# Optimization experiments

Measured on AMD Instinct MI355X. Metric: run time of the kernel, lower is better.

Reference implementation:

```python
import jax, jax.numpy as jnp
import numpy as np

NUM_HEADS = 16
DIM = 1024
B, L = 2, 2048
NEG = -10000000000.0


def setup_inputs() -> dict:
    key = jax.random.key(0)
    ks = jax.random.split(key, 8)
    queries = jax.random.normal(ks[0], (B, L, DIM), dtype=jnp.float32)
    keys = jax.random.normal(ks[1], (B, L, DIM), dtype=jnp.float32)
    values = jax.random.normal(ks[2], (B, L, DIM), dtype=jnp.float32)
    mask = jax.random.uniform(ks[3], (B, L, L)) < 0.1
    s = 1.0 / np.sqrt(DIM)
    Wq = jax.random.uniform(ks[4], (DIM, DIM), minval=-s, maxval=s, dtype=jnp.float32)
    Wk = jax.random.uniform(ks[5], (DIM, DIM), minval=-s, maxval=s, dtype=jnp.float32)
    Wv = jax.random.uniform(ks[6], (DIM, DIM), minval=-s, maxval=s, dtype=jnp.float32)
    Wo = jax.random.uniform(ks[7], (DIM, DIM), minval=-s, maxval=s, dtype=jnp.float32)
    return {"queries": queries, "keys": keys, "values": values, "mask": mask,
            "Wq": Wq, "Wk": Wk, "Wv": Wv, "Wo": Wo}


def reference(queries, keys, values, mask, Wq, Wk, Wv, Wo):
    b, l, d = queries.shape
    h = NUM_HEADS
    dk = d // h
    # torch Linear(bias=False): y = x @ W.T ; then view(b, l, dk, h) -> head axis LAST
    qs = (queries @ Wq.T).reshape(b, l, dk, h)
    ks = (keys @ Wk.T).reshape(b, l, dk, h)
    vs = (values @ Wv.T).reshape(b, l, dk, h)
    # routing is None in the live code path
    w = jnp.einsum('bidh,bodh->bioh', qs, ks) / jnp.sqrt(jnp.asarray(dk, jnp.float32))
    w = jnp.where(mask[..., None], NEG, w)          # masked_fill where mask True
    w = jax.nn.softmax(w, axis=-2)                   # softmax over key axis 'o'
    mha = jnp.einsum('bioh,bodh->bidh', w, vs).reshape(b, l, d)
    # dropout is identity in eval mode
    return mha @ Wo.T
```

## Files before the change

kernel.cpp:

```cpp
#include <hip/hip_runtime.h>
#include <hip/hip_bf16.h>
#include <cstdint>
#include <cstddef>

typedef unsigned short ushort_t;
typedef __attribute__((ext_vector_type(8))) short short8;
typedef __attribute__((ext_vector_type(8))) unsigned short ushort8;
typedef __attribute__((ext_vector_type(4))) unsigned short ushort4v;
typedef __attribute__((ext_vector_type(4))) float f32x4;
typedef __attribute__((ext_vector_type(2))) unsigned long long ull2;
typedef __attribute__((ext_vector_type(2))) unsigned int uint2v;

#define LPAD 72

#define PIPE_WAIT_BAR(N) do {                                              \
    asm volatile("s_waitcnt vmcnt(" #N ") lgkmcnt(0)" ::: "memory");       \
    __builtin_amdgcn_s_barrier();                                          \
    asm volatile("" ::: "memory");                                         \
} while (0)

__device__ __forceinline__ unsigned short f2bf(float f) {
    unsigned int x = __float_as_uint(f);
    unsigned int r = x + 0x7fffu + ((x >> 16) & 1u);
    return (unsigned short)(r >> 16);
}

__device__ __forceinline__ unsigned int cvt_pk_bf16(float lo, float hi) {
    unsigned int r;
    asm("v_cvt_pk_bf16_f32 %0, %1, %2" : "=v"(r) : "v"(lo), "v"(hi));
    return r;
}

__device__ __forceinline__ void async16(const ushort_t* g, ushort_t* l) {
    __builtin_amdgcn_global_load_lds(
        (const __attribute__((address_space(1))) unsigned int*)g,
        (__attribute__((address_space(3))) unsigned int*)l,
        16, 0, 0);
}

__global__ __launch_bounds__(256) void cvt(const float* __restrict__ q,
                                           const float* __restrict__ k,
                                           const float* __restrict__ v,
                                           const float* __restrict__ Wq,
                                           const float* __restrict__ Wk,
                                           const float* __restrict__ Wv,
                                           ushort_t* __restrict__ qb,
                                           ushort_t* __restrict__ kb,
                                           ushort_t* __restrict__ vb,
                                           ushort_t* __restrict__ Wqb,
                                           ushort_t* __restrict__ Wkb,
                                           ushort_t* __restrict__ Wvb) {
    const int z = blockIdx.y;
    const float* X = (z == 0) ? q : (z == 1) ? k : v;
    const float* W = (z == 0) ? Wq : (z == 1) ? Wk : Wv;
    ushort_t* Xo = (z == 0) ? qb : (z == 1) ? kb : vb;
    ushort_t* Wo2 = (z == 0) ? Wqb : (z == 1) ? Wkb : Wvb;
    const size_t idx = (((size_t)blockIdx.x << 8) + threadIdx.x) << 3;
    const float* src; ushort_t* dst; float sc = 1.0f;
    if (idx < 4194304) { src = X + idx; dst = Xo + idx; if (z == 0) sc = 0.125f; }
    else               { src = W + (idx - 4194304); dst = Wo2 + (idx - 4194304); }
    f32x4 a0 = *(const f32x4*)src, a1 = *(const f32x4*)(src + 4);
    ushort8 o;
    #pragma unroll
    for (int j = 0; j < 4; j++) { o[j] = f2bf(a0[j] * sc); o[j + 4] = f2bf(a1[j] * sc); }
    *(ushort8*)dst = o;
}

__global__ __launch_bounds__(256) void maskbits_kernel(const int* __restrict__ mask,
                                                       unsigned long long* __restrict__ Mbits) {
    const int row  = blockIdx.x;
    const int w    = threadIdx.x >> 6;
    const int lane = threadIdx.x & 63;
    const int* mrow = mask + (size_t)row * 2048;
    #pragma unroll
    for (int it = 0; it < 8; it++) {
        const int o = (it << 8) + (w << 6) + lane;
        const unsigned long long bb = __ballot(mrow[o] != 0);
        if (lane == 0) Mbits[(size_t)((it << 2) + w) * 4096 + row] = bb;
    }
}

__global__ __launch_bounds__(256) void woswz(const float* __restrict__ W,
                                             ushort_t* __restrict__ WoH) {
    __shared__ float row[1024 + 64];
    const int j = blockIdx.x, t = threadIdx.x;
    f32x4 v = *(const f32x4*)(W + (size_t)j * 1024 + (t << 2));
    #pragma unroll
    for (int s = 0; s < 4; s++) { const int c = (t << 2) + s; row[c + (c >> 4)] = v[s]; }
    __syncthreads();
    #pragma unroll
    for (int s = 0; s < 4; s++) {
        const int k = t + (s << 8);
        const int col = ((k & 63) << 4) + (k >> 6);
        WoH[(size_t)j * 1024 + k] = f2bf(row[col + (col >> 4)]);
    }
}

__global__ __launch_bounds__(256) void gemm_proj(const ushort_t* __restrict__ qb,
                                                 const ushort_t* __restrict__ kb,
                                                 const ushort_t* __restrict__ vb,
                                                 const ushort_t* __restrict__ Wqb,
                                                 const ushort_t* __restrict__ Wkb,
                                                 const ushort_t* __restrict__ Wvb,
                                                 ushort_t* __restrict__ Qh,
                                                 ushort_t* __restrict__ Kh,
                                                 ushort_t* __restrict__ VhT) {
    __shared__ ushort_t Xs[3][4096];
    __shared__ ushort_t Ws[3][4096];

    const int lid  = blockIdx.x;
    const int nIdx = lid / 96;
    const int rem  = lid % 96;
    const int z    = rem >> 5;
    const int mIdx = rem & 31;
    const int n0   = nIdx << 7;
    const int m0   = mIdx << 7;

    const ushort_t* Xb = (z == 0) ? qb : (z == 1) ? kb : vb;
    const ushort_t* Wb = (z == 0) ? Wqb : (z == 1) ? Wkb : Wvb;

    const int tid  = threadIdx.x;
    const int w    = tid >> 6;
    const int lane = tid & 63;
    const int lm   = lane & 15;
    const int quad = lane >> 4;
    const int wm   = w & 1;
    const int wn   = w >> 1;

    f32x4 acc[4][4];
    #pragma unroll
    for (int i = 0; i < 4; i++)
        #pragma unroll
        for (int j = 0; j < 4; j++) acc[i][j] = (f32x4){0.f, 0.f, 0.f, 0.f};

    auto stage = [&](int k0, int buf) {
        #pragma unroll
        for (int i = 0; i < 2; i++) {
            const int L   = (((w << 1) + i) << 6) + lane;
            const int c4  = L >> 7, row = L & 127;
            const int lb  = (((w << 1) + i) << 6) << 3;
            async16(Xb + (size_t)(m0 + row) * 1024 + k0 + (c4 << 3), &Xs[buf][lb]);
            async16(Wb + (size_t)(n0 + row) * 1024 + k0 + (c4 << 3), &Ws[buf][lb]);
        }
    };

    stage(0, 0);
    stage(32, 1);
    PIPE_WAIT_BAR(4);

    int cur = 0;
    for (int t = 0; t < 32; ++t) {
        int nb = cur + 2; if (nb >= 3) nb -= 3;
        if (t < 30) stage((t + 2) << 5, nb);
        short8 af[4], bf4[4];
        #pragma unroll
        for (int mf = 0; mf < 4; mf++)
            af[mf] = *(const short8*)&Xs[cur][((quad << 7) + (wm << 6) + (mf << 4) + lm) << 3];
        #pragma unroll
        for (int nf = 0; nf < 4; nf++)
            bf4[nf] = *(const short8*)&Ws[cur][((quad << 7) + (wn << 6) + (nf << 4) + lm) << 3];
        #pragma unroll
        for (int mf = 0; mf < 4; mf++)
            #pragma unroll
            for (int nf = 0; nf < 4; nf++)
                acc[mf][nf] = __builtin_amdgcn_mfma_f32_16x16x32_bf16(af[mf], bf4[nf], acc[mf][nf], 0, 0, 0);
        if (t < 30)       PIPE_WAIT_BAR(4);
        else if (t == 30) PIPE_WAIT_BAR(0);
        cur += 1; if (cur == 3) cur = 0;
    }

    const int bb    = m0 >> 11;
    const int l0    = m0 & 2047;
    const int dbase = (n0 >> 4) + (wn << 2);
    if (z != 2) {
        ushort_t* OUT = (z == 0) ? Qh : Kh;
        #pragma unroll
        for (int mf = 0; mf < 4; mf++)
            #pragma unroll
            for (int r = 0; r < 4; r++) {
                const int row = (wm << 6) + (mf << 4) + (quad << 2) + r;
                ushort4v o = { f2bf(acc[mf][0][r]), f2bf(acc[mf][1][r]),
                               f2bf(acc[mf][2][r]), f2bf(acc[mf][3][r]) };
                *(ushort4v*)(OUT + ((size_t)((bb << 4) + lm) * 2048 + l0 + row) * 64 + dbase) = o;
            }
    } else {
        #pragma unroll
        for (int mf = 0; mf < 4; mf++)
            #pragma unroll
            for (int nf = 0; nf < 4; nf++) {
                const int lbase = l0 + (wm << 6) + (mf << 4) + (quad << 2);
                ushort4v o = { f2bf(acc[mf][nf][0]), f2bf(acc[mf][nf][1]),
                               f2bf(acc[mf][nf][2]), f2bf(acc[mf][nf][3]) };
                *(ushort4v*)(VhT + ((size_t)((bb << 4) + lm) * 64 + dbase + nf) * 2048 + lbase) = o;
            }
    }
}

__global__ __launch_bounds__(256) void gemm_out(const ushort_t* __restrict__ mhaH,
                                                const ushort_t* __restrict__ WoH,
                                                float* __restrict__ C) {
    __shared__ ushort_t Xs[3][4096];
    __shared__ ushort_t Ws[3][2048];

    const int lid  = blockIdx.x;
    const int mIdx = ((lid & 7) << 2) | ((lid >> 3) & 3);
    const int nIdx = lid >> 5;
    const int m0   = mIdx << 7;
    const int n0   = nIdx << 6;

    const int tid  = threadIdx.x;
    const int w    = tid >> 6;
    const int lane = tid & 63;
    const int lm   = lane & 15;
    const int quad = lane >> 4;
    const int wm   = w & 1;
    const int wn   = w >> 1;
    const int ab   = m0 >> 11;
    const int al0  = m0 & 2047;

    f32x4 acc[4][2];
    #pragma unroll
    for (int i = 0; i < 4; i++)
        #pragma unroll
        for (int j = 0; j < 2; j++) acc[i][j] = (f32x4){0.f, 0.f, 0.f, 0.f};

    auto stage = [&](int k0, int buf) {
        const int h  = k0 >> 6;
        const int d0 = k0 & 63;
        #pragma unroll
        for (int i = 0; i < 2; i++) {
            const int L   = (i << 8) + (w << 6) + lane;
            const int c4  = L >> 7, row = L & 127;
            async16(mhaH + ((size_t)(ab * 16 + h) * 2048 + al0 + row) * 64 + d0 + (c4 << 3),
                    &Xs[buf][((i << 8) + (w << 6)) << 3]);
        }
        {
            const int L   = (w << 6) + lane;
            const int c4  = L >> 6, row = L & 63;
            async16(WoH + (size_t)(n0 + row) * 1024 + k0 + (c4 << 3),
                    &Ws[buf][(w << 6) << 3]);
        }
    };

    stage(0, 0);
    stage(32, 1);
    PIPE_WAIT_BAR(3);

    int cur = 0;
    for (int t = 0; t < 32; ++t) {
        int nb = cur + 2; if (nb >= 3) nb -= 3;
        if (t < 30) stage((t + 2) << 5, nb);
        short8 af[4], bf2[2];
        #pragma unroll
        for (int mf = 0; mf < 4; mf++)
            af[mf] = *(const short8*)&Xs[cur][((quad << 7) + (wm << 6) + (mf << 4) + lm) << 3];
        #pragma unroll
        for (int nf = 0; nf < 2; nf++)
            bf2[nf] = *(const short8*)&Ws[cur][((quad << 6) + (wn << 5) + (nf << 4) + lm) << 3];
        #pragma unroll
        for (int mf = 0; mf < 4; mf++)
            #pragma unroll
            for (int nf = 0; nf < 2; nf++)
                acc[mf][nf] = __builtin_amdgcn_mfma_f32_16x16x32_bf16(af[mf], bf2[nf], acc[mf][nf], 0, 0, 0);
        if (t < 30)       PIPE_WAIT_BAR(3);
        else if (t == 30) PIPE_WAIT_BAR(0);
        cur += 1; if (cur == 3) cur = 0;
    }
    #pragma unroll
    for (int mf = 0; mf < 4; mf++)
        #pragma unroll
        for (int nf = 0; nf < 2; nf++)
            #pragma unroll
            for (int r = 0; r < 4; r++) {
                const int row = m0 + (wm << 6) + (mf << 4) + (quad << 2) + r;
                const int col = n0 + (wn << 5) + (nf << 4) + lm;
                C[(size_t)row * 1024 + col] = acc[mf][nf][r];
            }
}

__global__ __launch_bounds__(256, 2) void flash_attn(const ushort_t* __restrict__ Qh,
                                                     const ushort_t* __restrict__ Kh,
                                                     const ushort_t* __restrict__ VhT,
                                                     const unsigned long long* __restrict__ Mbits,
                                                     ushort_t* __restrict__ mhaH) {
    __shared__ ushort_t Ks[3][4096];
    __shared__ ushort_t Vs[3][4096];
    __shared__ ushort_t Pw[4][2][16 * LPAD];

    const int tid  = threadIdx.x;
    const int w    = tid >> 6;
    const int lane = tid & 63;
    const int lm   = lane & 15;
    const int quad = lane >> 4;
    const int lid  = blockIdx.x;
    const int bh   = ((lid & 7) << 2) | ((lid >> 3) & 3);
    const int q0   = (lid >> 5) << 7;
    const int b    = bh >> 4;

    const ushort_t* Qb  = Qh  + ((size_t)bh << 17);
    const ushort_t* Kb  = Kh  + ((size_t)bh << 17);
    const ushort_t* Vtb = VhT + ((size_t)bh << 17);

    short8 aq[2][2];
    #pragma unroll
    for (int g = 0; g < 2; g++) {
        const ushort_t* qp = Qb + (size_t)(q0 + (w << 5) + (g << 4) + lm) * 64 + (quad << 3);
        aq[g][0] = *(const short8*)qp;
        aq[g][1] = *(const short8*)(qp + 32);
    }

    float l_part[2][4] = {{0.f,0.f,0.f,0.f},{0.f,0.f,0.f,0.f}};
    f32x4 o_acc[2][4] = {{{0.f,0.f,0.f,0.f},{0.f,0.f,0.f,0.f},{0.f,0.f,0.f,0.f},{0.f,0.f,0.f,0.f}},
                         {{0.f,0.f,0.f,0.f},{0.f,0.f,0.f,0.f},{0.f,0.f,0.f,0.f},{0.f,0.f,0.f,0.f}}};

    const int rowbase  = (b << 11) + q0 + (w << 5);
    const int shamt    = (lm & 7) << 2;
    const bool hi_half = lm >= 8;

    const ushort_t* ksrc = Kb  + (size_t)((lm << 2) + w) * 64 + (quad << 3);
    const ushort_t* vsrc = Vtb + (size_t)((w << 4) + lm) * 2048 + (quad << 3);

    auto stageKV = [&](int kt0, int buf) {
        async16(ksrc + (size_t)kt0 * 64,      &Ks[buf][((w << 7)     ) << 3]);
        async16(ksrc + (size_t)kt0 * 64 + 32, &Ks[buf][((w << 7) + 64) << 3]);
        async16(vsrc + kt0,      &Vs[buf][((w << 7)     ) << 3]);
        async16(vsrc + kt0 + 32, &Vs[buf][((w << 7) + 64) << 3]);
    };

    stageKV(0, 0);
    stageKV(64, 1);
    PIPE_WAIT_BAR(4);

    int cur = 0;
    for (int t = 0; t < 32; ++t) {
        const int kt0 = t << 6;
        int nb = cur + 2; if (nb >= 3) nb -= 3;

        const unsigned long long* Mt = Mbits + (size_t)(kt0 >> 6) * 4096 + rowbase;
        unsigned long long mb[2][4];
        #pragma unroll
        for (int g = 0; g < 2; g++) {
            const unsigned long long* mp = Mt + (g << 4) + (quad << 2);
            ull2 t0 = *(const ull2*)mp;
            ull2 t1 = *(const ull2*)(mp + 2);
            mb[g][0] = t0[0]; mb[g][1] = t0[1]; mb[g][2] = t1[0]; mb[g][3] = t1[1];
        }

        if (t < 30) stageKV(kt0 + 128, nb);

        short8 bk[4][2], bv[4][2];
        #pragma unroll
        for (int c = 0; c < 4; c++) {
            bk[c][0] = *(const short8*)&Ks[cur][((c << 7) + lane) << 3];
            bk[c][1] = *(const short8*)&Ks[cur][((c << 7) + 64 + lane) << 3];
            bv[c][0] = *(const short8*)&Vs[cur][((c << 7) + lane) << 3];
            bv[c][1] = *(const short8*)&Vs[cur][((c << 7) + 64 + lane) << 3];
        }

        f32x4 s[2][4];
        __builtin_amdgcn_s_setprio(1);
        #pragma unroll
        for (int g = 0; g < 2; g++)
            #pragma unroll
            for (int c = 0; c < 4; c++) {
                f32x4 zz = {0.f, 0.f, 0.f, 0.f};
                zz = __builtin_amdgcn_mfma_f32_16x16x32_bf16(aq[g][0], bk[c][0], zz, 0, 0, 0);
                zz = __builtin_amdgcn_mfma_f32_16x16x32_bf16(aq[g][1], bk[c][1], zz, 0, 0, 0);
                s[g][c] = zz;
            }
        __builtin_amdgcn_s_setprio(0);

        #pragma unroll
        for (int g = 0; g < 2; g++) {
            #pragma unroll
            for (int r = 0; r < 4; r++) {
                const unsigned long long m64 = mb[g][r];
                const unsigned word = hi_half ? (unsigned)(m64 >> 32) : (unsigned)m64;
                const unsigned nib  = (word >> shamt) & 0xFu;
                float p0 = __expf(s[g][0][r]); if (nib & 1u) p0 = 0.f;
                float p1 = __expf(s[g][1][r]); if (nib & 2u) p1 = 0.f;
                float p2 = __expf(s[g][2][r]); if (nib & 4u) p2 = 0.f;
                float p3 = __expf(s[g][3][r]); if (nib & 8u) p3 = 0.f;
                l_part[g][r] += (p0 + p1) + (p2 + p3);
                uint2v pv2;
                pv2[0] = cvt_pk_bf16(p0, p1);
                pv2[1] = cvt_pk_bf16(p2, p3);
                *(uint2v*)&Pw[w][g][((quad << 2) + r) * LPAD + (lm << 2)] = pv2;
            }
        }

        __builtin_amdgcn_s_setprio(1);
        #pragma unroll
        for (int g = 0; g < 2; g++) {
            short8 ap0 = *(const short8*)&Pw[w][g][lm * LPAD + (quad << 3)];
            short8 ap1 = *(const short8*)&Pw[w][g][lm * LPAD + 32 + (quad << 3)];
            #pragma unroll
            for (int cd = 0; cd < 4; cd++) {
                o_acc[g][cd] = __builtin_amdgcn_mfma_f32_16x16x32_bf16(ap0, bv[cd][0], o_acc[g][cd], 0, 0, 0);
                o_acc[g][cd] = __builtin_amdgcn_mfma_f32_16x16x32_bf16(ap1, bv[cd][1], o_acc[g][cd], 0, 0, 0);
            }
        }
        __builtin_amdgcn_s_setprio(0);

        if (t < 30)       PIPE_WAIT_BAR(4);
        else if (t == 30) PIPE_WAIT_BAR(0);
        cur += 1; if (cur == 3) cur = 0;
    }

    #pragma unroll
    for (int g = 0; g < 2; g++) {
        #pragma unroll
        for (int r = 0; r < 4; r++) {
            float l = l_part[g][r];
            l += __shfl_xor(l, 1, 64);
            l += __shfl_xor(l, 2, 64);
            l += __shfl_xor(l, 4, 64);
            l += __shfl_xor(l, 8, 64);
            const float inv_l = 1.0f / l;
            const int i = q0 + (w << 5) + (g << 4) + (quad << 2) + r;
            ushort_t* orow = mhaH + (((size_t)bh * 2048 + i) << 6);
            #pragma unroll
            for (int cd = 0; cd < 4; cd++)
                orow[(cd << 4) + lm] = f2bf(o_acc[g][cd][r] * inv_l);
        }
    }
}

extern "C" void kernel_launch(void* const* d_in, const int* in_sizes, int n_in,
                              void* d_out, int out_size, void* d_ws, size_t ws_size,
                              hipStream_t stream) {
    const float* q    = (const float*)d_in[0];
    const float* k    = (const float*)d_in[1];
    const float* v    = (const float*)d_in[2];
    const int*   mask = (const int*)d_in[3];
    const float* Wq   = (const float*)d_in[4];
    const float* Wk   = (const float*)d_in[5];
    const float* Wv   = (const float*)d_in[6];
    const float* Wo   = (const float*)d_in[7];
    float* out = (float*)d_out;

    ushort_t* qb   = (ushort_t*)d_ws;
    ushort_t* kb   = qb  + 4194304;
    ushort_t* vb   = kb  + 4194304;
    ushort_t* Wqb  = vb  + 4194304;
    ushort_t* Wkb  = Wqb + 1048576;
    ushort_t* Wvb  = Wkb + 1048576;
    ushort_t* Qh   = Wvb + 1048576;
    ushort_t* Kh   = Qh  + 4194304;
    ushort_t* VhT  = Kh  + 4194304;
    ushort_t* mhaH = qb;
    ushort_t* WoH  = kb;
    unsigned long long* Mbits = (unsigned long long*)(kb + 1048576);

    dim3 gb(256);
    cvt<<<dim3(2560, 3), gb, 0, stream>>>(q, k, v, Wq, Wk, Wv, qb, kb, vb, Wqb, Wkb, Wvb);
    gemm_proj<<<dim3(768), gb, 0, stream>>>(qb, kb, vb, Wqb, Wkb, Wvb, Qh, Kh, VhT);
    maskbits_kernel<<<dim3(4096), gb, 0, stream>>>(mask, Mbits);
    woswz<<<dim3(1024), gb, 0, stream>>>(Wo, WoH);
    flash_attn<<<dim3(512), gb, 0, stream>>>(Qh, Kh, VhT, Mbits, mhaH);
    gemm_out<<<dim3(512), gb, 0, stream>>>(mhaH, WoH, out);
}
```

Baseline: 311.7 us.

## Fuse fp32-to-bf16 activation conversion into projection GEMM and merge prep kernels

```diff
diff --git a/kernel.cpp b/kernel.cpp
--- a/kernel.cpp
+++ b/kernel.cpp
@@ -38,74 +38,66 @@
         16, 0, 0);
 }
 
-__global__ __launch_bounds__(256) void cvt(const float* __restrict__ q,
-                                           const float* __restrict__ k,
-                                           const float* __restrict__ v,
-                                           const float* __restrict__ Wq,
-                                           const float* __restrict__ Wk,
-                                           const float* __restrict__ Wv,
-                                           ushort_t* __restrict__ qb,
-                                           ushort_t* __restrict__ kb,
-                                           ushort_t* __restrict__ vb,
-                                           ushort_t* __restrict__ Wqb,
-                                           ushort_t* __restrict__ Wkb,
-                                           ushort_t* __restrict__ Wvb) {
-    const int z = blockIdx.y;
-    const float* X = (z == 0) ? q : (z == 1) ? k : v;
-    const float* W = (z == 0) ? Wq : (z == 1) ? Wk : Wv;
-    ushort_t* Xo = (z == 0) ? qb : (z == 1) ? kb : vb;
-    ushort_t* Wo2 = (z == 0) ? Wqb : (z == 1) ? Wkb : Wvb;
-    const size_t idx = (((size_t)blockIdx.x << 8) + threadIdx.x) << 3;
-    const float* src; ushort_t* dst; float sc = 1.0f;
-    if (idx < 4194304) { src = X + idx; dst = Xo + idx; if (z == 0) sc = 0.125f; }
-    else               { src = W + (idx - 4194304); dst = Wo2 + (idx - 4194304); }
-    f32x4 a0 = *(const f32x4*)src, a1 = *(const f32x4*)(src + 4);
-    ushort8 o;
-    #pragma unroll
-    for (int j = 0; j < 4; j++) { o[j] = f2bf(a0[j] * sc); o[j + 4] = f2bf(a1[j] * sc); }
-    *(ushort8*)dst = o;
-}
-
-__global__ __launch_bounds__(256) void maskbits_kernel(const int* __restrict__ mask,
-                                                       unsigned long long* __restrict__ Mbits) {
-    const int row  = blockIdx.x;
-    const int w    = threadIdx.x >> 6;
-    const int lane = threadIdx.x & 63;
-    const int* mrow = mask + (size_t)row * 2048;
-    #pragma unroll
-    for (int it = 0; it < 8; it++) {
-        const int o = (it << 8) + (w << 6) + lane;
-        const unsigned long long bb = __ballot(mrow[o] != 0);
-        if (lane == 0) Mbits[(size_t)((it << 2) + w) * 4096 + row] = bb;
-    }
-}
-
-__global__ __launch_bounds__(256) void woswz(const float* __restrict__ W,
-                                             ushort_t* __restrict__ WoH) {
-    __shared__ float row[1024 + 64];
-    const int j = blockIdx.x, t = threadIdx.x;
-    f32x4 v = *(const f32x4*)(W + (size_t)j * 1024 + (t << 2));
-    #pragma unroll
-    for (int s = 0; s < 4; s++) { const int c = (t << 2) + s; row[c + (c >> 4)] = v[s]; }
-    __syncthreads();
-    #pragma unroll
-    for (int s = 0; s < 4; s++) {
-        const int k = t + (s << 8);
-        const int col = ((k & 63) << 4) + (k >> 6);
-        WoH[(size_t)j * 1024 + k] = f2bf(row[col + (col >> 4)]);
-    }
-}
-
-__global__ __launch_bounds__(256) void gemm_proj(const ushort_t* __restrict__ qb,
-                                                 const ushort_t* __restrict__ kb,
-                                                 const ushort_t* __restrict__ vb,
+__global__ __launch_bounds__(256) void prep(const int* __restrict__ mask,
+                                            const float* __restrict__ Wq,
+                                            const float* __restrict__ Wk,
+                                            const float* __restrict__ Wv,
+                                            const float* __restrict__ Wo,
+                                            ushort_t* __restrict__ Wqb,
+                                            ushort_t* __restrict__ Wkb,
+                                            ushort_t* __restrict__ Wvb,
+                                            ushort_t* __restrict__ WoH,
+                                            unsigned long long* __restrict__ Mbits) {
+    __shared__ float srow[1024 + 64];
+    const int bid = blockIdx.x;
+    const int tid = threadIdx.x;
+    if (bid < 4096) {
+        const int row  = bid;
+        const int w    = tid >> 6;
+        const int lane = tid & 63;
+        const int* mrow = mask + (size_t)row * 2048;
+        #pragma unroll
+        for (int it = 0; it < 8; it++) {
+            const int o = (it << 8) + (w << 6) + lane;
+            const unsigned long long bb = __ballot(mrow[o] != 0);
+            if (lane == 0) Mbits[(size_t)((it << 2) + w) * 4096 + row] = bb;
+        }
+    } else if (bid < 5632) {
+        const int q    = bid - 4096;
+        const int wsel = q >> 9;
+        const float* W = (wsel == 0) ? Wq : (wsel == 1) ? Wk : Wv;
+        ushort_t* Wb   = (wsel == 0) ? Wqb : (wsel == 1) ? Wkb : Wvb;
+        const size_t idx = (((size_t)(q & 511) << 8) + tid) << 3;
+        f32x4 a0 = *(const f32x4*)(W + idx), a1 = *(const f32x4*)(W + idx + 4);
+        ushort8 o;
+        #pragma unroll
+        for (int j = 0; j < 4; j++) { o[j] = f2bf(a0[j]); o[j + 4] = f2bf(a1[j]); }
+        *(ushort8*)(Wb + idx) = o;
+    } else {
+        const int j = bid - 5632;
+        f32x4 v = *(const f32x4*)(Wo + (size_t)j * 1024 + (tid << 2));
+        #pragma unroll
+        for (int s = 0; s < 4; s++) { const int c = (tid << 2) + s; srow[c + (c >> 4)] = v[s]; }
+        __syncthreads();
+        #pragma unroll
+        for (int s = 0; s < 4; s++) {
+            const int k = tid + (s << 8);
+            const int col = ((k & 63) << 4) + (k >> 6);
+            WoH[(size_t)j * 1024 + k] = f2bf(srow[col + (col >> 4)]);
+        }
+    }
+}
+
+__global__ __launch_bounds__(256) void gemm_proj(const float* __restrict__ qf,
+                                                 const float* __restrict__ kf,
+                                                 const float* __restrict__ vf,
                                                  const ushort_t* __restrict__ Wqb,
                                                  const ushort_t* __restrict__ Wkb,
                                                  const ushort_t* __restrict__ Wvb,
                                                  ushort_t* __restrict__ Qh,
                                                  ushort_t* __restrict__ Kh,
                                                  ushort_t* __restrict__ VhT) {
-    __shared__ ushort_t Xs[3][4096];
+    __shared__ ushort_t Xs[2][4096];
     __shared__ ushort_t Ws[3][4096];
 
     const int lid  = blockIdx.x;
@@ -116,8 +108,9 @@
     const int n0   = nIdx << 7;
     const int m0   = mIdx << 7;
 
-    const ushort_t* Xb = (z == 0) ? qb : (z == 1) ? kb : vb;
+    const float* Xf = (z == 0) ? qf : (z == 1) ? kf : vf;
     const ushort_t* Wb = (z == 0) ? Wqb : (z == 1) ? Wkb : Wvb;
+    const float sc = (z == 0) ? 0.125f : 1.0f;
 
     const int tid  = threadIdx.x;
     const int w    = tid >> 6;
@@ -133,40 +126,71 @@
         #pragma unroll
         for (int j = 0; j < 4; j++) acc[i][j] = (f32x4){0.f, 0.f, 0.f, 0.f};
 
-    auto stage = [&](int k0, int buf) {
+    const float* xbase = Xf + (size_t)(m0 + lane) * 1024 + (w << 3);
+
+    auto loadX = [&](int k0, f32x4 xr[2][2]) {
         #pragma unroll
         for (int i = 0; i < 2; i++) {
-            const int L   = (((w << 1) + i) << 6) + lane;
-            const int c4  = L >> 7, row = L & 127;
-            const int lb  = (((w << 1) + i) << 6) << 3;
-            async16(Xb + (size_t)(m0 + row) * 1024 + k0 + (c4 << 3), &Xs[buf][lb]);
+            const float* sp = xbase + (size_t)(i << 6) * 1024 + k0;
+            xr[i][0] = *(const f32x4*)sp;
+            xr[i][1] = *(const f32x4*)(sp + 4);
+        }
+    };
+    auto writeX = [&](const f32x4 xr[2][2], int buf) {
+        #pragma unroll
+        for (int i = 0; i < 2; i++) {
+            ushort8 o;
+            #pragma unroll
+            for (int j = 0; j < 4; j++) {
+                o[j]     = f2bf(xr[i][0][j] * sc);
+                o[j + 4] = f2bf(xr[i][1][j] * sc);
+            }
+            const int L = (w << 7) + (i << 6) + lane;
+            *(ushort8*)&Xs[buf][L << 3] = o;
+        }
+    };
+    auto stageW = [&](int k0, int buf) {
+        #pragma unroll
+        for (int i = 0; i < 2; i++) {
+            const int L  = (((w << 1) + i) << 6) + lane;
+            const int c4 = L >> 7, row = L & 127;
+            const int lb = (((w << 1) + i) << 6) << 3;
             async16(Wb + (size_t)(n0 + row) * 1024 + k0 + (c4 << 3), &Ws[buf][lb]);
         }
     };
 
-    stage(0, 0);
-    stage(32, 1);
-    PIPE_WAIT_BAR(4);
-
-    int cur = 0;
+    {
+        f32x4 x0[2][2];
+        loadX(0, x0);
+        stageW(0, 0);
+        stageW(32, 1);
+        writeX(x0, 0);
+        PIPE_WAIT_BAR(2);
+    }
+
+    int wcur = 0;
     for (int t = 0; t < 32; ++t) {
-        int nb = cur + 2; if (nb >= 3) nb -= 3;
-        if (t < 30) stage((t + 2) << 5, nb);
+        f32x4 xr[2][2];
+        if (t < 31) loadX((t + 1) << 5, xr);
+        if (t < 30) { int nb = wcur + 2; if (nb >= 3) nb -= 3; stageW((t + 2) << 5, nb); }
+
         short8 af[4], bf4[4];
         #pragma unroll
         for (int mf = 0; mf < 4; mf++)
-            af[mf] = *(const short8*)&Xs[cur][((quad << 7) + (wm << 6) + (mf << 4) + lm) << 3];
+            af[mf] = *(const short8*)&Xs[t & 1][((quad << 7) + (wm << 6) + (mf << 4) + lm) << 3];
         #pragma unroll
         for (int nf = 0; nf < 4; nf++)
-            bf4[nf] = *(const short8*)&Ws[cur][((quad << 7) + (wn << 6) + (nf << 4) + lm) << 3];
+            bf4[nf] = *(const short8*)&Ws[wcur][((quad << 7) + (wn << 6) + (nf << 4) + lm) << 3];
         #pragma unroll
         for (int mf = 0; mf < 4; mf++)
             #pragma unroll
             for (int nf = 0; nf < 4; nf++)
                 acc[mf][nf] = __builtin_amdgcn_mfma_f32_16x16x32_bf16(af[mf], bf4[nf], acc[mf][nf], 0, 0, 0);
-        if (t < 30)       PIPE_WAIT_BAR(4);
+
+        if (t < 31) writeX(xr, (t + 1) & 1);
+        if (t < 30)       PIPE_WAIT_BAR(2);
         else if (t == 30) PIPE_WAIT_BAR(0);
-        cur += 1; if (cur == 3) cur = 0;
+        wcur += 1; if (wcur == 3) wcur = 0;
     }
 
     const int bb    = m0 >> 11;
@@ -439,24 +463,19 @@
     const float* Wo   = (const float*)d_in[7];
     float* out = (float*)d_out;
 
-    ushort_t* qb   = (ushort_t*)d_ws;
-    ushort_t* kb   = qb  + 4194304;
-    ushort_t* vb   = kb  + 4194304;
-    ushort_t* Wqb  = vb  + 4194304;
+    ushort_t* Wqb  = (ushort_t*)d_ws;
     ushort_t* Wkb  = Wqb + 1048576;
     ushort_t* Wvb  = Wkb + 1048576;
-    ushort_t* Qh   = Wvb + 1048576;
+    ushort_t* WoH  = Wvb + 1048576;
+    unsigned long long* Mbits = (unsigned long long*)(WoH + 1048576);
+    ushort_t* Qh   = WoH + 1048576 + 524288;
     ushort_t* Kh   = Qh  + 4194304;
     ushort_t* VhT  = Kh  + 4194304;
-    ushort_t* mhaH = qb;
-    ushort_t* WoH  = kb;
-    unsigned long long* Mbits = (unsigned long long*)(kb + 1048576);
+    ushort_t* mhaH = VhT + 4194304;
 
     dim3 gb(256);
-    cvt<<<dim3(2560, 3), gb, 0, stream>>>(q, k, v, Wq, Wk, Wv, qb, kb, vb, Wqb, Wkb, Wvb);
-    gemm_proj<<<dim3(768), gb, 0, stream>>>(qb, kb, vb, Wqb, Wkb, Wvb, Qh, Kh, VhT);
-    maskbits_kernel<<<dim3(4096), gb, 0, stream>>>(mask, Mbits);
-    woswz<<<dim3(1024), gb, 0, stream>>>(Wo, WoH);
+    prep<<<dim3(6656), gb, 0, stream>>>(mask, Wq, Wk, Wv, Wo, Wqb, Wkb, Wvb, WoH, Mbits);
+    gemm_proj<<<dim3(768), gb, 0, stream>>>(q, k, v, Wqb, Wkb, Wvb, Qh, Kh, VhT);
     flash_attn<<<dim3(512), gb, 0, stream>>>(Qh, Kh, VhT, Mbits, mhaH);
     gemm_out<<<dim3(512), gb, 0, stream>>>(mhaH, WoH, out);
 }
```

Measured after the change: 326.6 us. 1.05x slower.

## Enlarge projection GEMM tiles to 256x256 and merge prep kernels

Applied to the files above, without the earlier changes.

```diff
diff --git a/kernel.cpp b/kernel.cpp
--- a/kernel.cpp
+++ b/kernel.cpp
@@ -38,27 +38,35 @@
         16, 0, 0);
 }
 
-__global__ __launch_bounds__(256) void cvt(const float* __restrict__ q,
-                                           const float* __restrict__ k,
-                                           const float* __restrict__ v,
-                                           const float* __restrict__ Wq,
-                                           const float* __restrict__ Wk,
-                                           const float* __restrict__ Wv,
-                                           ushort_t* __restrict__ qb,
-                                           ushort_t* __restrict__ kb,
-                                           ushort_t* __restrict__ vb,
-                                           ushort_t* __restrict__ Wqb,
-                                           ushort_t* __restrict__ Wkb,
-                                           ushort_t* __restrict__ Wvb) {
-    const int z = blockIdx.y;
-    const float* X = (z == 0) ? q : (z == 1) ? k : v;
-    const float* W = (z == 0) ? Wq : (z == 1) ? Wk : Wv;
-    ushort_t* Xo = (z == 0) ? qb : (z == 1) ? kb : vb;
-    ushort_t* Wo2 = (z == 0) ? Wqb : (z == 1) ? Wkb : Wvb;
-    const size_t idx = (((size_t)blockIdx.x << 8) + threadIdx.x) << 3;
+__global__ __launch_bounds__(256) void prep1(const float* __restrict__ q,
+                                             const float* __restrict__ k,
+                                             const float* __restrict__ v,
+                                             const float* __restrict__ Wq,
+                                             const float* __restrict__ Wk,
+                                             const float* __restrict__ Wv,
+                                             ushort_t* __restrict__ qb,
+                                             ushort_t* __restrict__ kb,
+                                             ushort_t* __restrict__ vb,
+                                             ushort_t* __restrict__ Wqb,
+                                             ushort_t* __restrict__ Wkb,
+                                             ushort_t* __restrict__ Wvb) {
+    const int bid = blockIdx.x;
+    const int tid = threadIdx.x;
     const float* src; ushort_t* dst; float sc = 1.0f;
-    if (idx < 4194304) { src = X + idx; dst = Xo + idx; if (z == 0) sc = 0.125f; }
-    else               { src = W + (idx - 4194304); dst = Wo2 + (idx - 4194304); }
+    if (bid < 6144) {
+        const int z   = bid >> 11;
+        const int blk = bid & 2047;
+        const size_t idx = (((size_t)blk << 8) + tid) << 3;
+        src = ((z == 0) ? q : (z == 1) ? k : v) + idx;
+        dst = ((z == 0) ? qb : (z == 1) ? kb : vb) + idx;
+        if (z == 0) sc = 0.125f;
+    } else {
+        const int qq   = bid - 6144;
+        const int wsel = qq >> 9;
+        const size_t idx = (((size_t)(qq & 511) << 8) + tid) << 3;
+        src = ((wsel == 0) ? Wq : (wsel == 1) ? Wk : Wv) + idx;
+        dst = ((wsel == 0) ? Wqb : (wsel == 1) ? Wkb : Wvb) + idx;
+    }
     f32x4 a0 = *(const f32x4*)src, a1 = *(const f32x4*)(src + 4);
     ushort8 o;
     #pragma unroll
@@ -66,55 +74,58 @@
     *(ushort8*)dst = o;
 }
 
-__global__ __launch_bounds__(256) void maskbits_kernel(const int* __restrict__ mask,
-                                                       unsigned long long* __restrict__ Mbits) {
-    const int row  = blockIdx.x;
-    const int w    = threadIdx.x >> 6;
-    const int lane = threadIdx.x & 63;
-    const int* mrow = mask + (size_t)row * 2048;
-    #pragma unroll
-    for (int it = 0; it < 8; it++) {
-        const int o = (it << 8) + (w << 6) + lane;
-        const unsigned long long bb = __ballot(mrow[o] != 0);
-        if (lane == 0) Mbits[(size_t)((it << 2) + w) * 4096 + row] = bb;
-    }
-}
-
-__global__ __launch_bounds__(256) void woswz(const float* __restrict__ W,
-                                             ushort_t* __restrict__ WoH) {
-    __shared__ float row[1024 + 64];
-    const int j = blockIdx.x, t = threadIdx.x;
-    f32x4 v = *(const f32x4*)(W + (size_t)j * 1024 + (t << 2));
-    #pragma unroll
-    for (int s = 0; s < 4; s++) { const int c = (t << 2) + s; row[c + (c >> 4)] = v[s]; }
-    __syncthreads();
-    #pragma unroll
-    for (int s = 0; s < 4; s++) {
-        const int k = t + (s << 8);
-        const int col = ((k & 63) << 4) + (k >> 6);
-        WoH[(size_t)j * 1024 + k] = f2bf(row[col + (col >> 4)]);
-    }
-}
-
-__global__ __launch_bounds__(256) void gemm_proj(const ushort_t* __restrict__ qb,
-                                                 const ushort_t* __restrict__ kb,
-                                                 const ushort_t* __restrict__ vb,
-                                                 const ushort_t* __restrict__ Wqb,
-                                                 const ushort_t* __restrict__ Wkb,
-                                                 const ushort_t* __restrict__ Wvb,
-                                                 ushort_t* __restrict__ Qh,
-                                                 ushort_t* __restrict__ Kh,
-                                                 ushort_t* __restrict__ VhT) {
-    __shared__ ushort_t Xs[3][4096];
-    __shared__ ushort_t Ws[3][4096];
+__global__ __launch_bounds__(256) void prep2(const int* __restrict__ mask,
+                                             const float* __restrict__ Wo,
+                                             ushort_t* __restrict__ WoH,
+                                             unsigned long long* __restrict__ Mbits) {
+    __shared__ float srow[1024 + 64];
+    const int bid = blockIdx.x;
+    const int tid = threadIdx.x;
+    if (bid < 4096) {
+        const int row  = bid;
+        const int w    = tid >> 6;
+        const int lane = tid & 63;
+        const int* mrow = mask + (size_t)row * 2048;
+        #pragma unroll
+        for (int it = 0; it < 8; it++) {
+            const int o = (it << 8) + (w << 6) + lane;
+            const unsigned long long bb = __ballot(mrow[o] != 0);
+            if (lane == 0) Mbits[(size_t)((it << 2) + w) * 4096 + row] = bb;
+        }
+    } else {
+        const int j = bid - 4096;
+        f32x4 v = *(const f32x4*)(Wo + (size_t)j * 1024 + (tid << 2));
+        #pragma unroll
+        for (int s = 0; s < 4; s++) { const int c = (tid << 2) + s; srow[c + (c >> 4)] = v[s]; }
+        __syncthreads();
+        #pragma unroll
+        for (int s = 0; s < 4; s++) {
+            const int k = tid + (s << 8);
+            const int col = ((k & 63) << 4) + (k >> 6);
+            WoH[(size_t)j * 1024 + k] = f2bf(srow[col + (col >> 4)]);
+        }
+    }
+}
+
+__global__ __launch_bounds__(512, 2) void gemm_proj(const ushort_t* __restrict__ qb,
+                                                    const ushort_t* __restrict__ kb,
+                                                    const ushort_t* __restrict__ vb,
+                                                    const ushort_t* __restrict__ Wqb,
+                                                    const ushort_t* __restrict__ Wkb,
+                                                    const ushort_t* __restrict__ Wvb,
+                                                    ushort_t* __restrict__ Qh,
+                                                    ushort_t* __restrict__ Kh,
+                                                    ushort_t* __restrict__ VhT) {
+    __shared__ ushort_t Xs[3][8192];
+    __shared__ ushort_t Ws[3][8192];
 
     const int lid  = blockIdx.x;
-    const int nIdx = lid / 96;
-    const int rem  = lid % 96;
-    const int z    = rem >> 5;
-    const int mIdx = rem & 31;
-    const int n0   = nIdx << 7;
-    const int m0   = mIdx << 7;
+    const int nIdx = lid / 48;
+    const int rem  = lid % 48;
+    const int z    = rem >> 4;
+    const int mIdx = rem & 15;
+    const int n0   = nIdx << 8;
+    const int m0   = mIdx << 8;
 
     const ushort_t* Xb = (z == 0) ? qb : (z == 1) ? kb : vb;
     const ushort_t* Wb = (z == 0) ? Wqb : (z == 1) ? Wkb : Wvb;
@@ -127,9 +138,9 @@
     const int wm   = w & 1;
     const int wn   = w >> 1;
 
-    f32x4 acc[4][4];
-    #pragma unroll
-    for (int i = 0; i < 4; i++)
+    f32x4 acc[8][4];
+    #pragma unroll
+    for (int i = 0; i < 8; i++)
         #pragma unroll
         for (int j = 0; j < 4; j++) acc[i][j] = (f32x4){0.f, 0.f, 0.f, 0.f};
 
@@ -137,7 +148,7 @@
         #pragma unroll
         for (int i = 0; i < 2; i++) {
             const int L   = (((w << 1) + i) << 6) + lane;
-            const int c4  = L >> 7, row = L & 127;
+            const int c4  = L >> 8, row = L & 255;
             const int lb  = (((w << 1) + i) << 6) << 3;
             async16(Xb + (size_t)(m0 + row) * 1024 + k0 + (c4 << 3), &Xs[buf][lb]);
             async16(Wb + (size_t)(n0 + row) * 1024 + k0 + (c4 << 3), &Ws[buf][lb]);
@@ -152,15 +163,15 @@
     for (int t = 0; t < 32; ++t) {
         int nb = cur + 2; if (nb >= 3) nb -= 3;
         if (t < 30) stage((t + 2) << 5, nb);
-        short8 af[4], bf4[4];
-        #pragma unroll
-        for (int mf = 0; mf < 4; mf++)
-            af[mf] = *(const short8*)&Xs[cur][((quad << 7) + (wm << 6) + (mf << 4) + lm) << 3];
+        short8 af[8], bf4[4];
+        #pragma unroll
+        for (int mf = 0; mf < 8; mf++)
+            af[mf] = *(const short8*)&Xs[cur][((quad << 8) + (wm << 7) + (mf << 4) + lm) << 3];
         #pragma unroll
         for (int nf = 0; nf < 4; nf++)
-            bf4[nf] = *(const short8*)&Ws[cur][((quad << 7) + (wn << 6) + (nf << 4) + lm) << 3];
-        #pragma unroll
-        for (int mf = 0; mf < 4; mf++)
+            bf4[nf] = *(const short8*)&Ws[cur][((quad << 8) + (wn << 6) + (nf << 4) + lm) << 3];
+        #pragma unroll
+        for (int mf = 0; mf < 8; mf++)
             #pragma unroll
             for (int nf = 0; nf < 4; nf++)
                 acc[mf][nf] = __builtin_amdgcn_mfma_f32_16x16x32_bf16(af[mf], bf4[nf], acc[mf][nf], 0, 0, 0);
@@ -175,20 +186,20 @@
     if (z != 2) {
         ushort_t* OUT = (z == 0) ? Qh : Kh;
         #pragma unroll
-        for (int mf = 0; mf < 4; mf++)
+        for (int mf = 0; mf < 8; mf++)
             #pragma unroll
             for (int r = 0; r < 4; r++) {
-                const int row = (wm << 6) + (mf << 4) + (quad << 2) + r;
+                const int row = (wm << 7) + (mf << 4) + (quad << 2) + r;
                 ushort4v o = { f2bf(acc[mf][0][r]), f2bf(acc[mf][1][r]),
                                f2bf(acc[mf][2][r]), f2bf(acc[mf][3][r]) };
                 *(ushort4v*)(OUT + ((size_t)((bb << 4) + lm) * 2048 + l0 + row) * 64 + dbase) = o;
             }
     } else {
         #pragma unroll
-        for (int mf = 0; mf < 4; mf++)
+        for (int mf = 0; mf < 8; mf++)
             #pragma unroll
             for (int nf = 0; nf < 4; nf++) {
-                const int lbase = l0 + (wm << 6) + (mf << 4) + (quad << 2);
+                const int lbase = l0 + (wm << 7) + (mf << 4) + (quad << 2);
                 ushort4v o = { f2bf(acc[mf][nf][0]), f2bf(acc[mf][nf][1]),
                                f2bf(acc[mf][nf][2]), f2bf(acc[mf][nf][3]) };
                 *(ushort4v*)(VhT + ((size_t)((bb << 4) + lm) * 64 + dbase + nf) * 2048 + lbase) = o;
@@ -453,10 +464,9 @@
     unsigned long long* Mbits = (unsigned long long*)(kb + 1048576);
 
     dim3 gb(256);
-    cvt<<<dim3(2560, 3), gb, 0, stream>>>(q, k, v, Wq, Wk, Wv, qb, kb, vb, Wqb, Wkb, Wvb);
-    gemm_proj<<<dim3(768), gb, 0, stream>>>(qb, kb, vb, Wqb, Wkb, Wvb, Qh, Kh, VhT);
-    maskbits_kernel<<<dim3(4096), gb, 0, stream>>>(mask, Mbits);
-    woswz<<<dim3(1024), gb, 0, stream>>>(Wo, WoH);
+    prep1<<<dim3(7680), gb, 0, stream>>>(q, k, v, Wq, Wk, Wv, qb, kb, vb, Wqb, Wkb, Wvb);
+    gemm_proj<<<dim3(192), dim3(512), 0, stream>>>(qb, kb, vb, Wqb, Wkb, Wvb, Qh, Kh, VhT);
+    prep2<<<dim3(5120), gb, 0, stream>>>(mask, Wo, WoH, Mbits);
     flash_attn<<<dim3(512), gb, 0, stream>>>(Qh, Kh, VhT, Mbits, mhaH);
     gemm_out<<<dim3(512), gb, 0, stream>>>(mhaH, WoH, out);
 }
```

New measurement: 303.8 us. 2.5% less time.
